# Kernel optimization log

Measured on AMD Instinct MI355X. Metric: run time of the kernel, lower is better.

Reference implementation:

```python
import jax, jax.numpy as jnp
import numpy as np

DIM_INPUT = 100000
DIM_LATENT = 128
NNZ = 819200
BATCH = 16384


def setup_inputs() -> dict:
    key = jax.random.key(0)
    k1, k2, k3, k4, k5 = jax.random.split(key, 5)
    vals = jax.random.uniform(k1, (NNZ,), dtype=jnp.float32)
    row_idx = jnp.sort(jax.random.randint(k2, (NNZ,), 0, BATCH, dtype=jnp.int32))
    col_idx = jax.random.randint(k3, (NNZ,), 0, DIM_INPUT, dtype=jnp.int32)
    # learned parameters (match torch init: w0 zeros, w/v randn)
    w0 = jnp.zeros((1,), dtype=jnp.float32)
    w = jax.random.normal(k4, (DIM_INPUT,), dtype=jnp.float32)
    v = jax.random.normal(k5, (DIM_INPUT, DIM_LATENT), dtype=jnp.float32)
    return {"vals": vals, "row_idx": row_idx, "col_idx": col_idx,
            "batch": BATCH, "w0": w0, "w": w, "v": v}


def reference(vals, row_idx, col_idx, batch, w0, w, v):
    # x is a sparse [batch, dim_input] matrix in COO form (row_idx, col_idx, vals).
    # linear term: w0 + x @ w
    linear = w0[0] + jax.ops.segment_sum(vals * w[col_idx], row_idx,
                                         num_segments=batch)
    # gather latent rows once: [nnz, K]
    v_rows = v[col_idx]
    weighted = vals[:, None] * v_rows                      # [nnz, K]
    xv = jax.ops.segment_sum(weighted, row_idx, num_segments=batch)       # [B, K]
    x_v_sq = jax.ops.segment_sum(weighted * v_rows, row_idx,
                                 num_segments=batch)       # x @ (v**2): [B, K]
    interaction = 0.5 * (jnp.sum(xv * xv, axis=1) - jnp.sum(x_v_sq, axis=1))
    return linear + interaction
```

## Files before the change

### kernel.cpp

```cpp
#include <hip/hip_runtime.h>

#define FM_NNZ   819200
#define FM_BATCH 16384
#define FM_DIM   100000
#define FM_K     128
#define NB_SHIFT 13
#define NBUCK    13
#define GBATCH   8


static __device__ __forceinline__ uint32_t f2bf(float f) {
    uint32_t u = __float_as_uint(f);
    return (u + 0x7fffu + ((u >> 16) & 1u)) >> 16;
}

__global__ __launch_bounds__(256) void cvt_kernel(const float* __restrict__ v,
                                                  uint32_t* __restrict__ vb) {
    const float4* __restrict__ v4 = (const float4*)v;
    uint2* __restrict__ o = (uint2*)vb;
    const int n = (FM_DIM * FM_K) / 4;
    for (int i = blockIdx.x * blockDim.x + threadIdx.x; i < n;
         i += gridDim.x * blockDim.x) {
        const float4 x = v4[i];
        uint2 r;
        r.x = f2bf(x.x) | (f2bf(x.y) << 16);
        r.y = f2bf(x.z) | (f2bf(x.w) << 16);
        o[i] = r;
    }
}


__global__ __launch_bounds__(256, 8) void fm_fwd_kernel(
    const float* __restrict__ vals,
    const int*   __restrict__ row_idx,
    const int*   __restrict__ col_idx,
    const float* __restrict__ w0,
    const float* __restrict__ w_,
    const uint32_t* __restrict__ vb,
    float*       __restrict__ out)
{
    __shared__ uint2 lists[4][2][128];

    const int wave = threadIdx.x >> 6;
    const int lane = threadIdx.x & 63;
    const int wid  = blockIdx.x * 4 + wave;
    const int row0 = 2 * wid;

    int s[3];
    #pragma unroll
    for (int q = 0; q < 3; ++q) {
        const int key = row0 + q;
        int lo = 0, hi = FM_NNZ;
        while (lo < hi) {
            const int mid = (lo + hi) >> 1;
            if (row_idx[mid] < key) lo = mid + 1; else hi = mid;
        }
        s[q] = lo;
    }
    const int s0 = s[0], s1 = s[1], s2 = s[2];

    int cA, cB, cC, cD;  float aA, aB, aC, aD;  int bA, bB, bC, bD;
    {
        int idx, ic; bool ok;
        idx = s0 + lane;      ok = idx < s1; ic = min(idx, FM_NNZ - 1);
        cA = col_idx[ic]; aA = ok ? vals[ic] : 0.f; bA = ok ? (cA >> NB_SHIFT) : 127;
        idx = s0 + 64 + lane; ok = idx < s1; ic = min(idx, FM_NNZ - 1);
        cB = col_idx[ic]; aB = ok ? vals[ic] : 0.f; bB = ok ? (cB >> NB_SHIFT) : 127;
        idx = s1 + lane;      ok = idx < s2; ic = min(idx, FM_NNZ - 1);
        cC = col_idx[ic]; aC = ok ? vals[ic] : 0.f; bC = ok ? (cC >> NB_SHIFT) : 127;
        idx = s1 + 64 + lane; ok = idx < s2; ic = min(idx, FM_NNZ - 1);
        cD = col_idx[ic]; aD = ok ? vals[ic] : 0.f; bD = ok ? (cD >> NB_SHIFT) : 127;
    }

    float lin0 = aA * w_[cA] + aB * w_[cB];
    float lin1 = aC * w_[cC] + aD * w_[cD];

    const unsigned long long lt = (1ull << lane) - 1ull;
    int total0, total1;
    {
        int posA = -1, posB = -1, run = 0;
        for (int p = 0; p < NBUCK; ++p) {
            const unsigned long long mA = __ballot(bA == p);
            const unsigned long long mB = __ballot(bB == p);
            const int nA = __popcll(mA);
            if (bA == p) posA = run + __popcll(mA & lt);
            if (bB == p) posB = run + nA + __popcll(mB & lt);
            run += nA + __popcll(mB);
        }
        total0 = run;
        if (posA >= 0) lists[wave][0][posA] = make_uint2((uint32_t)cA, __float_as_uint(aA));
        if (posB >= 0) lists[wave][0][posB] = make_uint2((uint32_t)cB, __float_as_uint(aB));
    }
    {
        int posC = -1, posD = -1, run = 0;
        for (int p = 0; p < NBUCK; ++p) {
            const unsigned long long mC = __ballot(bC == p);
            const unsigned long long mD = __ballot(bD == p);
            const int nC = __popcll(mC);
            if (bC == p) posC = run + __popcll(mC & lt);
            if (bD == p) posD = run + nC + __popcll(mD & lt);
            run += nC + __popcll(mD);
        }
        total1 = run;
        if (posC >= 0) lists[wave][1][posC] = make_uint2((uint32_t)cC, __float_as_uint(aC));
        if (posD >= 0) lists[wave][1][posD] = make_uint2((uint32_t)cD, __float_as_uint(aD));
    }
    __syncthreads();

    float xv0l = 0.f, xv0h = 0.f, sq0l = 0.f, sq0h = 0.f;
    float xv1l = 0.f, xv1h = 0.f, sq1l = 0.f, sq1h = 0.f;

#define ROWWALK(r, total, xvl, xvh, sql, sqh)                                 \
    for (int i = 0; i < (total); i += GBATCH) {                               \
        uint2    ca[GBATCH];                                                  \
        uint32_t vv[GBATCH];                                                  \
        _Pragma("unroll")                                                     \
        for (int u = 0; u < GBATCH; ++u) {                                    \
            const int e = min(i + u, (total) - 1);                            \
            ca[u] = lists[wave][r][e];             \
        }                                                                     \
        _Pragma("unroll")                                                     \
        for (int u = 0; u < GBATCH; ++u) {                                    \
            vv[u] = vb[(size_t)ca[u].x * 64 + lane];  \
        }                                                                     \
        _Pragma("unroll")                                                     \
        for (int u = 0; u < GBATCH; ++u) {                                    \
            const float aj  = (i + u < (total)) ? __uint_as_float(ca[u].y) : 0.f; \
            const float vlo = __uint_as_float(vv[u] << 16);                   \
            const float vhi = __uint_as_float(vv[u] & 0xffff0000u);           \
            const float tl = aj * vlo, th = aj * vhi;                         \
            xvl += tl;  xvh += th;                                            \
            sql = fmaf(tl, vlo, sql);  sqh = fmaf(th, vhi, sqh);              \
        }                                                                     \
    }

    ROWWALK(0, total0, xv0l, xv0h, sq0l, sq0h)
    ROWWALK(1, total1, xv1l, xv1h, sq1l, sq1h)
#undef ROWWALK

    float part0 = xv0l * xv0l + xv0h * xv0h - sq0l - sq0h;
    float part1 = xv1l * xv1l + xv1h * xv1h - sq1l - sq1h;
    #pragma unroll
    for (int off = 32; off > 0; off >>= 1) {
        part0 += __shfl_down(part0, off);
        part1 += __shfl_down(part1, off);
        lin0  += __shfl_down(lin0,  off);
        lin1  += __shfl_down(lin1,  off);
    }
    if (lane == 0) {
        const float bias = w0[0];
        out[row0]     = bias + lin0 + 0.5f * part0;
        out[row0 + 1] = bias + lin1 + 0.5f * part1;
    }
}

extern "C" void kernel_launch(void* const* d_in, const int* in_sizes, int n_in,
                              void* d_out, int out_size, void* d_ws, size_t ws_size,
                              hipStream_t stream) {
    const float* vals    = (const float*)d_in[0];
    const int*   row_idx = (const int*)  d_in[1];
    const int*   col_idx = (const int*)  d_in[2];
    const float* w0      = (const float*)d_in[4];
    const float* w       = (const float*)d_in[5];
    const float* v       = (const float*)d_in[6];
    float*       out     = (float*)d_out;
    uint32_t*    vb      = (uint32_t*)d_ws;

    cvt_kernel<<<1024, 256, 0, stream>>>(v, vb);
    fm_fwd_kernel<<<FM_BATCH / 8, 256, 0, stream>>>(
        vals, row_idx, col_idx, w0, w, vb, out);
}
```

Measured before the change: 149.8 us.

## Gather four latent rows per wave with 16-byte loads and finer column buckets

```diff
diff --git a/kernel.cpp b/kernel.cpp
--- a/kernel.cpp
+++ b/kernel.cpp
@@ -4,9 +4,9 @@
 #define FM_BATCH 16384
 #define FM_DIM   100000
 #define FM_K     128
-#define NB_SHIFT 13
-#define NBUCK    13
-#define GBATCH   8
+#define NB_SHIFT 12
+#define NBUCK    25
+#define UNR      4
 
 
 static __device__ __forceinline__ uint32_t f2bf(float f) {
@@ -43,6 +43,8 @@
 
     const int wave = threadIdx.x >> 6;
     const int lane = threadIdx.x & 63;
+    const int grp  = lane >> 4;
+    const int ql   = lane & 15;
     const int wid  = blockIdx.x * 4 + wave;
     const int row0 = 2 * wid;
 
@@ -107,39 +109,61 @@
     }
     __syncthreads();
 
-    float xv0l = 0.f, xv0h = 0.f, sq0l = 0.f, sq0h = 0.f;
-    float xv1l = 0.f, xv1h = 0.f, sq1l = 0.f, sq1h = 0.f;
+    const uint4* __restrict__ vb4 = (const uint4*)vb;
 
-#define ROWWALK(r, total, xvl, xvh, sql, sqh)                                 \
-    for (int i = 0; i < (total); i += GBATCH) {                               \
-        uint2    ca[GBATCH];                                                  \
-        uint32_t vv[GBATCH];                                                  \
+    float xv[8], sq[8];
+    float part0, part1;
+
+#define ROWWALK(r, total, partr)                                              \
+    {                                                                         \
         _Pragma("unroll")                                                     \
-        for (int u = 0; u < GBATCH; ++u) {                                    \
-            const int e = min(i + u, (total) - 1);                            \
-            ca[u] = lists[wave][r][e];             \
+        for (int d = 0; d < 8; ++d) { xv[d] = 0.f; sq[d] = 0.f; }             \
+        for (int i = 0; i < (total); i += 4 * UNR) {                          \
+            uint2 ca[UNR];                                                    \
+            uint4 vv[UNR];                                                    \
+            _Pragma("unroll")                                                 \
+            for (int u = 0; u < UNR; ++u) {                                   \
+                const int e = min(i + 4 * u + grp, (total) - 1);              \
+                ca[u] = lists[wave][r][e];       \
+            }                                                                 \
+            _Pragma("unroll")                                                 \
+            for (int u = 0; u < UNR; ++u) {                                   \
+                vv[u] = vb4[(size_t)ca[u].x * 16 + ql];        \
+            }                                                                 \
+            __builtin_amdgcn_sched_barrier(0);                                \
+            _Pragma("unroll")                                                 \
+            for (int u = 0; u < UNR; ++u) {                                   \
+                const float aj = (i + 4 * u + grp < (total))                  \
+                                     ? __uint_as_float(ca[u].y) : 0.f;        \
+                const uint32_t wd[4] = {vv[u].x, vv[u].y, vv[u].z, vv[u].w};  \
+                _Pragma("unroll")                                             \
+                for (int q2 = 0; q2 < 4; ++q2) {                              \
+                    const float vlo = __uint_as_float(wd[q2] << 16);          \
+                    const float vhi = __uint_as_float(wd[q2] & 0xffff0000u);  \
+                    const float tl = aj * vlo, th = aj * vhi;                 \
+                    xv[2*q2]   += tl;                                         \
+                    xv[2*q2+1] += th;                                         \
+                    sq[2*q2]   = fmaf(tl, vlo, sq[2*q2]);                     \
+                    sq[2*q2+1] = fmaf(th, vhi, sq[2*q2+1]);                   \
+                }                                                             \
+            }                                                                 \
         }                                                                     \
+        float px = 0.f, sqs = 0.f;                                            \
         _Pragma("unroll")                                                     \
-        for (int u = 0; u < GBATCH; ++u) {                                    \
-            vv[u] = vb[(size_t)ca[u].x * 64 + lane];  \
+        for (int d = 0; d < 8; ++d) {                                         \
+            float t = xv[d];                                                  \
+            t += __shfl_xor(t, 16);                                           \
+            t += __shfl_xor(t, 32);                \
+            px = fmaf(t, t, px);                                              \
+            sqs += sq[d];                                                     \
         }                                                                     \
-        _Pragma("unroll")                                                     \
-        for (int u = 0; u < GBATCH; ++u) {                                    \
-            const float aj  = (i + u < (total)) ? __uint_as_float(ca[u].y) : 0.f; \
-            const float vlo = __uint_as_float(vv[u] << 16);                   \
-            const float vhi = __uint_as_float(vv[u] & 0xffff0000u);           \
-            const float tl = aj * vlo, th = aj * vhi;                         \
-            xvl += tl;  xvh += th;                                            \
-            sql = fmaf(tl, vlo, sql);  sqh = fmaf(th, vhi, sqh);              \
-        }                                                                     \
+        partr = ((lane < 16) ? px : 0.f) - sqs;    \
     }
 
-    ROWWALK(0, total0, xv0l, xv0h, sq0l, sq0h)
-    ROWWALK(1, total1, xv1l, xv1h, sq1l, sq1h)
+    ROWWALK(0, total0, part0)
+    ROWWALK(1, total1, part1)
 #undef ROWWALK
 
-    float part0 = xv0l * xv0l + xv0h * xv0h - sq0l - sq0h;
-    float part1 = xv1l * xv1l + xv1h * xv1h - sq1l - sq1h;
     #pragma unroll
     for (int off = 32; off > 0; off >>= 1) {
         part0 += __shfl_down(part0, off);
```

After: 197.7 us. 31.9% more time.
